# Kernel optimization log

Measured on AMD Instinct MI355X. Metric: run time of the kernel, lower is better.

## Reference

```python
import jax, jax.numpy as jnp
import numpy as np

E = 384      # hidden_dim
H = 8        # num_attention_heads
D = E // H   # head_dim = 48


def setup_inputs() -> dict:
    key = jax.random.key(0)
    ks = jax.random.split(key, 11)
    B, S = 4, 2048
    patch_embeds = jax.random.normal(ks[0], (B, S, E), dtype=jnp.float32)
    attention_mask = jax.random.randint(ks[1], (B, S), 0, 2).astype(bool)
    s = 1.0 / np.sqrt(E)
    Wq = jax.random.normal(ks[2], (E, E), dtype=jnp.float32) * s
    bq = jnp.zeros((E,), dtype=jnp.float32)
    Wk = jax.random.normal(ks[3], (E, E), dtype=jnp.float32) * s
    bk = jnp.zeros((E,), dtype=jnp.float32)
    Wv = jax.random.normal(ks[4], (E, E), dtype=jnp.float32) * s
    bv = jnp.zeros((E,), dtype=jnp.float32)
    Wo = jax.random.normal(ks[5], (E, E), dtype=jnp.float32) * s
    bo = jnp.zeros((E,), dtype=jnp.float32)
    return {"patch_embeds": patch_embeds, "attention_mask": attention_mask,
            "Wq": Wq, "bq": bq, "Wk": Wk, "bk": bk,
            "Wv": Wv, "bv": bv, "Wo": Wo, "bo": bo}


def reference(patch_embeds, attention_mask, Wq, bq, Wk, bk, Wv, bv, Wo, bo):
    B, S, _ = patch_embeds.shape
    scale = D ** (-0.5)
    # QKV projections (nn.Linear: x @ W.T + b); W stored as [out,in]
    q = patch_embeds @ Wq.T + bq
    k = patch_embeds @ Wk.T + bk
    v = patch_embeds @ Wv.T + bv
    # [B,S,E] -> [B,H,S,D]
    q = q.reshape(B, S, H, D).transpose(0, 2, 1, 3)
    k = k.reshape(B, S, H, D).transpose(0, 2, 1, 3)
    v = v.reshape(B, S, H, D).transpose(0, 2, 1, 3)
    # scaled dot-product attention with key mask (True = masked)
    scores = jnp.einsum('bhqd,bhkd->bhqk', q, k) * scale
    mask = attention_mask[:, None, None, :]  # [B,1,1,S]
    scores = jnp.where(mask, -jnp.inf, scores)
    weights = jax.nn.softmax(scores, axis=-1)
    out = jnp.einsum('bhqk,bhkd->bhqd', weights, v)
    out = out.transpose(0, 2, 1, 3).reshape(B, S, E)
    return out @ Wo.T + bo
```

## Files before the change

### kernel.cpp

```cpp
#include <hip/hip_runtime.h>
#include <math.h>

#define B_ 4
#define S_ 2048
#define E_ 384
#define H_ 8
#define D_ 48
#define M_ (B_*S_)
#define DP_ 64
constexpr float QK_SCALE = 0.14433756729740643f * 1.4426950408889634f;

typedef __attribute__((ext_vector_type(8))) short short8;
typedef __attribute__((ext_vector_type(4))) float f32x4;
typedef unsigned short u16;

__device__ inline u16 f2bf(float f) {
    unsigned u = __float_as_uint(f);
    return (u16)((u + 0x7FFFu + ((u >> 16) & 1u)) >> 16);
}
__device__ inline float bf2f(u16 h) { return __uint_as_float(((unsigned)h) << 16); }
__device__ inline unsigned pk2(float a, float b) {
    return (unsigned)f2bf(a) | ((unsigned)f2bf(b) << 16);
}
__device__ inline unsigned pk2_fast(float a, float b) {
#if __has_builtin(__builtin_amdgcn_perm)
    unsigned ua = __float_as_uint(a) + 0x8000u;
    unsigned ub = __float_as_uint(b) + 0x8000u;
    return __builtin_amdgcn_perm(ub, ua, 0x07060302u);
#else
    return pk2(a, b);
#endif
}
__device__ inline float fexp2(float x) {
#if __has_builtin(__builtin_amdgcn_exp2f)
    return __builtin_amdgcn_exp2f(x);
#else
    return exp2f(x);
#endif
}
__device__ inline void glld16(const void* g, void* l) {
    __builtin_amdgcn_global_load_lds((const __attribute__((address_space(1))) unsigned int*)g,
                                     (__attribute__((address_space(3))) unsigned int*)l, 16, 0, 0);
}

__global__ __launch_bounds__(256) void prep(const float4* __restrict__ x,
                                            const int* __restrict__ mask,
                                            const float4* __restrict__ wq,
                                            const float4* __restrict__ wk,
                                            const float4* __restrict__ wv,
                                            const float4* __restrict__ wo,
                                            uint2* __restrict__ xb,
                                            uint2* __restrict__ wb,
                                            u16* __restrict__ Qp, u16* __restrict__ Kp) {
    const int bx = blockIdx.x, t = threadIdx.x;
    if (bx < 3072) {
        int i = bx * 256 + t;
        float4 v = x[i];
        uint2 H;
        H.x = pk2(v.x, v.y);
        H.y = pk2(v.z, v.w);
        xb[i] = H;
    } else if (bx < 3072 + 144) {
        int i = (bx - 3072) * 256 + t;
        const int n4 = 36864;
        const float4* srcs[4] = {wq, wk, wv, wo};
        #pragma unroll
        for (int j = 0; j < 4; ++j) {
            float4 v = srcs[j][i];
            uint2 H;
            H.x = pk2(v.x, v.y);
            H.y = pk2(v.z, v.w);
            wb[(size_t)j * n4 + i] = H;
        }
    } else {
        int i = (bx - 3216) * 256 + t;
        int bh = i >> 11, s = i & 2047, b = bh >> 3;
        size_t off = ((size_t)bh * S_ + s) * DP_ + 48;
        uint4 qz = {0x00004300u, 0, 0, 0};
        uint4 kz = {mask[b * S_ + s] ? 0x0000BF80u : 0u, 0, 0, 0};
        uint4 z  = {0, 0, 0, 0};
        *reinterpret_cast<uint4*>(Qp + off)     = qz;
        *reinterpret_cast<uint4*>(Qp + off + 8) = z;
        *reinterpret_cast<uint4*>(Kp + off)     = kz;
        *reinterpret_cast<uint4*>(Kp + off + 8) = z;
    }
}

__global__ __launch_bounds__(256) void gemm_qkv3(const u16* __restrict__ xb,
                                                 const u16* __restrict__ wb,
                                                 const float* __restrict__ bq,
                                                 const float* __restrict__ bk,
                                                 const float* __restrict__ bv,
                                                 u16* __restrict__ Qp, u16* __restrict__ Kp,
                                                 u16* __restrict__ Vtp) {
    __shared__ u16 smem[4 * 4096];
    u16* As = smem;

    const int t = threadIdx.x, w = t >> 6, lane = t & 63;
    const int ln = lane & 15, quad = lane >> 4;
    const int gr = lane >> 3;
    const int gc = (lane & 7) ^ gr;
    const int m0 = blockIdx.x * 64;
    const int n0 = blockIdx.y * 64;
    const int b  = m0 >> 11;

    f32x4 acc[3][4];
    #pragma unroll
    for (int j = 0; j < 3; ++j)
        #pragma unroll
        for (int nt = 0; nt < 4; ++nt)
            acc[j][nt] = (f32x4){0.f, 0.f, 0.f, 0.f};

    for (int kk = 0; kk < 384; kk += 64) {
        __syncthreads();
        #pragma unroll
        for (int i = 0; i < 2; ++i) {
            int r0 = w * 16 + i * 8;
            glld16(xb + (size_t)(m0 + r0 + gr) * E_ + kk + gc * 8, As + r0 * 64);
        }
        #pragma unroll
        for (int j = 0; j < 3; ++j)
            #pragma unroll
            for (int i = 0; i < 2; ++i) {
                int r0 = w * 16 + i * 8;
                glld16(wb + (size_t)j * 147456 + (size_t)(n0 + r0 + gr) * E_ + kk + gc * 8,
                       smem + (1 + j) * 4096 + r0 * 64);
            }
        __syncthreads();

        #pragma unroll
        for (int ks = 0; ks < 2; ++ks) {
            const int slot = (ks * 4 + quad) ^ (ln & 7);
            short8 ah = *reinterpret_cast<const short8*>(&As[(w * 16 + ln) * 64 + slot * 8]);
            #pragma unroll
            for (int j = 0; j < 3; ++j) {
                const u16* Wsj = smem + (1 + j) * 4096;
                #pragma unroll
                for (int nt = 0; nt < 4; ++nt) {
                    short8 wf = *reinterpret_cast<const short8*>(&Wsj[(nt * 16 + ln) * 64 + slot * 8]);
                    acc[j][nt] = __builtin_amdgcn_mfma_f32_16x16x32_bf16(ah, wf, acc[j][nt], 0, 0, 0);
                }
            }
        }
    }

    {
        const int s_base = (m0 & 2047) + w * 16 + quad * 4;
        #pragma unroll
        for (int nt = 0; nt < 4; ++nt) {
            const int col = n0 + nt * 16 + ln;
            const int h   = (col * 683) >> 15;
            const int d   = col - h * 48;
            const float bc = bv[col];
            u16* dst = Vtp + ((size_t)(b * 8 + h) * 48 + d) * 2048;
            uint2 pk;
            pk.x = pk2(acc[2][nt][0] + bc, acc[2][nt][1] + bc);
            pk.y = pk2(acc[2][nt][2] + bc, acc[2][nt][3] + bc);
            *reinterpret_cast<uint2*>(dst + s_base) = pk;
        }
    }

    u16* TrQ = smem;
    u16* TrK = smem + 64 * 76;
    __syncthreads();
    #pragma unroll
    for (int nt = 0; nt < 4; ++nt) {
        const int col = n0 + nt * 16 + ln;
        const float bcq = bq[col], bck = bk[col];
        #pragma unroll
        for (int r = 0; r < 4; ++r) {
            int row = w * 16 + quad * 4 + r;
            TrQ[row * 76 + nt * 16 + ln] = f2bf((acc[0][nt][r] + bcq) * QK_SCALE);
            TrK[row * 76 + nt * 16 + ln] = f2bf(acc[1][nt][r] + bck);
        }
    }
    __syncthreads();
    {
        const int row = t >> 2, quarter = t & 3;
        const int s   = (m0 & 2047) + row;
        #pragma unroll
        for (int c = 0; c < 2; ++c) {
            int gcol = n0 + quarter * 16 + c * 8;
            int h = (gcol * 683) >> 15;
            int d = gcol - h * 48;
            size_t off = ((size_t)(b * 8 + h) * 2048 + s) * DP_ + d;
            *reinterpret_cast<uint4*>(Qp + off) =
                *reinterpret_cast<const uint4*>(&TrQ[row * 76 + quarter * 16 + c * 8]);
            *reinterpret_cast<uint4*>(Kp + off) =
                *reinterpret_cast<const uint4*>(&TrK[row * 76 + quarter * 16 + c * 8]);
        }
    }
}

__global__ __launch_bounds__(256) void gemm_out(const u16* __restrict__ ab,
                                                const u16* __restrict__ wb,
                                                const float* __restrict__ bo, float* __restrict__ out) {
    __shared__ u16 smem[2 * 4096 + 2 * 4096];
    u16* As = smem;
    u16* Ws = smem + 2 * 4096;
    const int t = threadIdx.x, w = t >> 6, lane = t & 63;
    const int ln = lane & 15, quad = lane >> 4;
    const int gr = lane >> 3;
    const int gc = (lane & 7) ^ gr;
    const int m0 = blockIdx.x * 64, n0 = blockIdx.y * 64;
    const u16* wh = wb + (size_t)3 * 147456;

    f32x4 acc[4];
    #pragma unroll
    for (int nt = 0; nt < 4; ++nt) acc[nt] = (f32x4){0.f, 0.f, 0.f, 0.f};

    auto stage = [&](int bf, int kk) {
        #pragma unroll
        for (int i = 0; i < 2; ++i) {
            int r0 = w * 16 + i * 8;
            glld16(ab + (size_t)(m0 + r0 + gr) * E_ + kk + gc * 8, As + bf * 4096 + r0 * 64);
            glld16(wh + (size_t)(n0 + r0 + gr) * E_ + kk + gc * 8, Ws + bf * 4096 + r0 * 64);
        }
    };

    stage(0, 0);
    __syncthreads();
    #pragma unroll
    for (int it = 0; it < 6; ++it) {
        const int cur = it & 1;
        if (it < 5) stage(cur ^ 1, (it + 1) * 64);
        const u16* Ab = As + cur * 4096;
        const u16* Wb = Ws + cur * 4096;
        #pragma unroll
        for (int ks = 0; ks < 2; ++ks) {
            const int slot = (ks * 4 + quad) ^ (ln & 7);
            short8 ah = *reinterpret_cast<const short8*>(&Ab[(w * 16 + ln) * 64 + slot * 8]);
            #pragma unroll
            for (int nt = 0; nt < 4; ++nt) {
                short8 wf = *reinterpret_cast<const short8*>(&Wb[(nt * 16 + ln) * 64 + slot * 8]);
                acc[nt] = __builtin_amdgcn_mfma_f32_16x16x32_bf16(ah, wf, acc[nt], 0, 0, 0);
            }
        }
        __syncthreads();
    }

    #pragma unroll
    for (int nt = 0; nt < 4; ++nt) {
        const int col = n0 + nt * 16 + ln;
        const float bc = bo[col];
        #pragma unroll
        for (int r = 0; r < 4; ++r) {
            size_t row = (size_t)(m0 + w * 16 + quad * 4 + r);
            out[row * E_ + col] = acc[nt][r] + bc;
        }
    }
}

__global__ __launch_bounds__(256, 2) void attn_mfma(const u16* __restrict__ Qp,
                                                    const u16* __restrict__ Kp,
                                                    const u16* __restrict__ Vtp,
                                                    u16* __restrict__ AO) {
    __shared__ __align__(16) u16 QPs[128 * 64];
    __shared__ __align__(16) u16 Ksh[2][64 * 64];
    __shared__ __align__(16) u16 Vt[2][48 * 64];
    __shared__ float linv[4][32];

    const int t    = threadIdx.x;
    const int w    = t >> 6;
    const int lane = t & 63;
    const int ln   = lane & 15;
    const int quad = lane >> 4;
    const int gr   = lane >> 3;
    const int gc   = (lane & 7) ^ gr;
    const int bh   = blockIdx.x;
    const int q0   = blockIdx.y * 128;
    const int b    = bh >> 3, h = bh & 7;
    const int cb   = h * 48;
    const size_t rb = (size_t)b * S_;

    const u16* Qsrc = Qp  + ((size_t)bh * S_ + q0) * DP_;
    const u16* Ksrc = Kp  + (size_t)bh * S_ * DP_;
    const u16* Vsrc = Vtp + (size_t)bh * 48 * 2048;

    const int swz0 = ((quad    ) ^ (ln & 7)) << 3;
    const int swz1 = ((4 + quad) ^ (ln & 7)) << 3;
    const u16* kA[2][2], *vA[2][2];
    #pragma unroll
    for (int bf = 0; bf < 2; ++bf) {
        kA[bf][0] = &Ksh[bf][ln * 64 + swz0];
        kA[bf][1] = &Ksh[bf][ln * 64 + swz1];
        vA[bf][0] = &Vt[bf][ln * 64 + swz0];
        vA[bf][1] = &Vt[bf][ln * 64 + swz1];
    }
    int qrow[2];
    const u16 *pR[2][2];
    u16* pW[2][4];
    #pragma unroll
    for (int qt = 0; qt < 2; ++qt) {
        qrow[qt] = (w * 32 + qt * 16 + ln) * 64;
        pR[qt][0] = &QPs[qrow[qt] + swz0];
        pR[qt][1] = &QPs[qrow[qt] + swz1];
        #pragma unroll
        for (int Mt = 0; Mt < 4; ++Mt)
            pW[qt][Mt] = &QPs[qrow[qt] +
                ((((Mt * 2 + (quad >> 1)) ^ (ln & 7)) << 3) | ((quad & 1) << 2))];
    }

    auto stage = [&](int bf, int kt) {
        const int k0 = kt * 64;
        glld16(Ksrc + (size_t)(k0 + w * 16 + gr) * DP_ + gc * 8,     &Ksh[bf][(w * 16) * 64]);
        glld16(Ksrc + (size_t)(k0 + w * 16 + 8 + gr) * DP_ + gc * 8, &Ksh[bf][(w * 16 + 8) * 64]);
        if (w < 3) {
            glld16(Vsrc + (size_t)(w * 16 + gr) * 2048 + k0 + gc * 8,     &Vt[bf][(w * 16) * 64]);
            glld16(Vsrc + (size_t)(w * 16 + 8 + gr) * 2048 + k0 + gc * 8, &Vt[bf][(w * 16 + 8) * 64]);
        }
    };

    #pragma unroll
    for (int i = 0; i < 4; ++i) {
        int r0 = w * 32 + i * 8;
        glld16(Qsrc + (size_t)(r0 + gr) * DP_ + gc * 8, &QPs[r0 * 64]);
    }
    stage(0, 0);
    __syncthreads();

    short8 qf[2][2];
    #pragma unroll
    for (int qt = 0; qt < 2; ++qt) {
        qf[qt][0] = *reinterpret_cast<const short8*>(pR[qt][0]);
        qf[qt][1] = *reinterpret_cast<const short8*>(pR[qt][1]);
    }

    f32x4 o[2][3];
    #pragma unroll
    for (int qt = 0; qt < 2; ++qt)
        #pragma unroll
        for (int nt = 0; nt < 3; ++nt) o[qt][nt] = (f32x4){0.f, 0.f, 0.f, 0.f};
    float lq[2] = {0.f, 0.f};

    auto body = [&](int cur, int nxt, int ktn) {
        if (ktn < 32) stage(nxt, ktn);

        f32x4 sc[4][2];
        #pragma unroll
        for (int Mt = 0; Mt < 4; ++Mt) {
            short8 kf0 = *reinterpret_cast<const short8*>(kA[cur][0] + Mt * 1024);
            short8 kf1 = *reinterpret_cast<const short8*>(kA[cur][1] + Mt * 1024);
            #pragma unroll
            for (int qt = 0; qt < 2; ++qt) {
                f32x4 a0 = __builtin_amdgcn_mfma_f32_16x16x32_bf16(kf0, qf[qt][0], (f32x4){0.f,0.f,0.f,0.f}, 0, 0, 0);
                sc[Mt][qt] = __builtin_amdgcn_mfma_f32_16x16x32_bf16(kf1, qf[qt][1], a0, 0, 0, 0);
            }
        }

        #pragma unroll
        for (int qt = 0; qt < 2; ++qt)
            #pragma unroll
            for (int Mt = 0; Mt < 4; ++Mt) {
                float p0 = fexp2(sc[Mt][qt][0]);
                float p1 = fexp2(sc[Mt][qt][1]);
                float p2 = fexp2(sc[Mt][qt][2]);
                float p3 = fexp2(sc[Mt][qt][3]);
                lq[qt] += (p0 + p1) + (p2 + p3);
                uint2 pk;
                pk.x = pk2_fast(p0, p1);
                pk.y = pk2_fast(p2, p3);
                *reinterpret_cast<uint2*>(pW[qt][Mt]) = pk;
            }

        short8 pa[2][2];
        #pragma unroll
        for (int qt = 0; qt < 2; ++qt) {
            pa[qt][0] = *reinterpret_cast<const short8*>(pR[qt][0]);
            pa[qt][1] = *reinterpret_cast<const short8*>(pR[qt][1]);
        }
        #pragma unroll
        for (int nt = 0; nt < 3; ++nt) {
            short8 vb0 = *reinterpret_cast<const short8*>(vA[cur][0] + nt * 1024);
            short8 vb1 = *reinterpret_cast<const short8*>(vA[cur][1] + nt * 1024);
            #pragma unroll
            for (int qt = 0; qt < 2; ++qt) {
                o[qt][nt] = __builtin_amdgcn_mfma_f32_16x16x32_bf16(pa[qt][0], vb0, o[qt][nt], 0, 0, 0);
                o[qt][nt] = __builtin_amdgcn_mfma_f32_16x16x32_bf16(pa[qt][1], vb1, o[qt][nt], 0, 0, 0);
            }
        }
        __syncthreads();
    };

    for (int kt = 0; kt < 32; kt += 2) {
        body(0, 1, kt + 1);
        body(1, 0, kt + 2);
    }

    #pragma unroll
    for (int qt = 0; qt < 2; ++qt) {
        float l = lq[qt];
        l += __shfl_xor(l, 16);
        l += __shfl_xor(l, 32);
        if (quad == 0) linv[w][qt * 16 + ln] = 1.0f / l;
    }
    __syncthreads();
    #pragma unroll
    for (int qt = 0; qt < 2; ++qt) {
        f32x4 il = *reinterpret_cast<const f32x4*>(&linv[w][qt * 16 + quad * 4]);
        #pragma unroll
        for (int nt = 0; nt < 3; ++nt)
            #pragma unroll
            for (int r = 0; r < 4; ++r) {
                size_t row = rb + q0 + w * 32 + qt * 16 + quad * 4 + r;
                size_t idx = row * E_ + cb + nt * 16 + ln;
                AO[idx] = f2bf(o[qt][nt][r] * il[r]);
            }
    }
}

extern "C" void kernel_launch(void* const* d_in, const int* in_sizes, int n_in,
                              void* d_out, int out_size, void* d_ws, size_t ws_size,
                              hipStream_t stream) {
    (void)in_sizes; (void)n_in; (void)out_size; (void)ws_size;
    const float* x    = (const float*)d_in[0];
    const int*   mask = (const int*)  d_in[1];
    const float* Wq   = (const float*)d_in[2];
    const float* bq   = (const float*)d_in[3];
    const float* Wk   = (const float*)d_in[4];
    const float* bk   = (const float*)d_in[5];
    const float* Wv   = (const float*)d_in[6];
    const float* bv   = (const float*)d_in[7];
    const float* Wo   = (const float*)d_in[8];
    const float* bo   = (const float*)d_in[9];

    const size_t NELEM = (size_t)M_ * E_;
    const size_t WELEM = (size_t)E_ * E_;
    const size_t PEL   = (size_t)B_ * H_ * S_ * DP_;
    u16* ws = (u16*)d_ws;
    u16* xb  = ws;
    u16* wb  = xb + NELEM;
    u16* Qp  = wb + 4 * WELEM;
    u16* Kp  = Qp + PEL;
    u16* Vtp = Kp + PEL;
    u16* AO  = xb;

    dim3 blk(256);
    prep<<<dim3(3472), blk, 0, stream>>>(
        (const float4*)x, mask,
        (const float4*)Wq, (const float4*)Wk, (const float4*)Wv, (const float4*)Wo,
        (uint2*)xb, (uint2*)wb, Qp, Kp);

    gemm_qkv3<<<dim3(M_ / 64, 6), blk, 0, stream>>>(xb, wb, bq, bk, bv, Qp, Kp, Vtp);

    attn_mfma<<<dim3(B_ * H_, S_ / 128), blk, 0, stream>>>(Qp, Kp, Vtp, AO);

    gemm_out<<<dim3(M_ / 64, 6), blk, 0, stream>>>(AO, wb, bo, (float*)d_out);
}
```

Measured before the change: 145.1 us.

## Split attention block across 8 waves with 16 query rows each

Result: slower. 148.9 us (+2.6%).

```diff
diff --git a/kernel.cpp b/kernel.cpp
--- a/kernel.cpp
+++ b/kernel.cpp
@@ -251,14 +251,14 @@
     }
 }
 
-__global__ __launch_bounds__(256, 2) void attn_mfma(const u16* __restrict__ Qp,
+__global__ __launch_bounds__(512, 4) void attn_mfma(const u16* __restrict__ Qp,
                                                     const u16* __restrict__ Kp,
                                                     const u16* __restrict__ Vtp,
                                                     u16* __restrict__ AO) {
     __shared__ __align__(16) u16 QPs[128 * 64];
     __shared__ __align__(16) u16 Ksh[2][64 * 64];
     __shared__ __align__(16) u16 Vt[2][48 * 64];
-    __shared__ float linv[4][32];
+    __shared__ float linv[8][16];
 
     const int t    = threadIdx.x;
     const int w    = t >> 6;
@@ -287,97 +287,74 @@
         vA[bf][0] = &Vt[bf][ln * 64 + swz0];
         vA[bf][1] = &Vt[bf][ln * 64 + swz1];
     }
-    int qrow[2];
-    const u16 *pR[2][2];
-    u16* pW[2][4];
-    #pragma unroll
-    for (int qt = 0; qt < 2; ++qt) {
-        qrow[qt] = (w * 32 + qt * 16 + ln) * 64;
-        pR[qt][0] = &QPs[qrow[qt] + swz0];
-        pR[qt][1] = &QPs[qrow[qt] + swz1];
-        #pragma unroll
-        for (int Mt = 0; Mt < 4; ++Mt)
-            pW[qt][Mt] = &QPs[qrow[qt] +
-                ((((Mt * 2 + (quad >> 1)) ^ (ln & 7)) << 3) | ((quad & 1) << 2))];
-    }
+    const int qrow = (w * 16 + ln) * 64;
+    const u16* pR[2];
+    u16* pW[4];
+    pR[0] = &QPs[qrow + swz0];
+    pR[1] = &QPs[qrow + swz1];
+    #pragma unroll
+    for (int Mt = 0; Mt < 4; ++Mt)
+        pW[Mt] = &QPs[qrow +
+            ((((Mt * 2 + (quad >> 1)) ^ (ln & 7)) << 3) | ((quad & 1) << 2))];
 
     auto stage = [&](int bf, int kt) {
         const int k0 = kt * 64;
-        glld16(Ksrc + (size_t)(k0 + w * 16 + gr) * DP_ + gc * 8,     &Ksh[bf][(w * 16) * 64]);
-        glld16(Ksrc + (size_t)(k0 + w * 16 + 8 + gr) * DP_ + gc * 8, &Ksh[bf][(w * 16 + 8) * 64]);
-        if (w < 3) {
-            glld16(Vsrc + (size_t)(w * 16 + gr) * 2048 + k0 + gc * 8,     &Vt[bf][(w * 16) * 64]);
-            glld16(Vsrc + (size_t)(w * 16 + 8 + gr) * 2048 + k0 + gc * 8, &Vt[bf][(w * 16 + 8) * 64]);
-        }
+        glld16(Ksrc + (size_t)(k0 + w * 8 + gr) * DP_ + gc * 8, &Ksh[bf][(w * 8) * 64]);
+        if (w < 6)
+            glld16(Vsrc + (size_t)(w * 8 + gr) * 2048 + k0 + gc * 8, &Vt[bf][(w * 8) * 64]);
     };
 
     #pragma unroll
-    for (int i = 0; i < 4; ++i) {
-        int r0 = w * 32 + i * 8;
+    for (int i = 0; i < 2; ++i) {
+        int r0 = w * 16 + i * 8;
         glld16(Qsrc + (size_t)(r0 + gr) * DP_ + gc * 8, &QPs[r0 * 64]);
     }
     stage(0, 0);
     __syncthreads();
 
-    short8 qf[2][2];
-    #pragma unroll
-    for (int qt = 0; qt < 2; ++qt) {
-        qf[qt][0] = *reinterpret_cast<const short8*>(pR[qt][0]);
-        qf[qt][1] = *reinterpret_cast<const short8*>(pR[qt][1]);
-    }
-
-    f32x4 o[2][3];
-    #pragma unroll
-    for (int qt = 0; qt < 2; ++qt)
-        #pragma unroll
-        for (int nt = 0; nt < 3; ++nt) o[qt][nt] = (f32x4){0.f, 0.f, 0.f, 0.f};
-    float lq[2] = {0.f, 0.f};
+    short8 qf[2];
+    qf[0] = *reinterpret_cast<const short8*>(pR[0]);
+    qf[1] = *reinterpret_cast<const short8*>(pR[1]);
+
+    f32x4 o[3];
+    #pragma unroll
+    for (int nt = 0; nt < 3; ++nt) o[nt] = (f32x4){0.f, 0.f, 0.f, 0.f};
+    float lq = 0.f;
 
     auto body = [&](int cur, int nxt, int ktn) {
         if (ktn < 32) stage(nxt, ktn);
 
-        f32x4 sc[4][2];
+        f32x4 sc[4];
         #pragma unroll
         for (int Mt = 0; Mt < 4; ++Mt) {
             short8 kf0 = *reinterpret_cast<const short8*>(kA[cur][0] + Mt * 1024);
             short8 kf1 = *reinterpret_cast<const short8*>(kA[cur][1] + Mt * 1024);
-            #pragma unroll
-            for (int qt = 0; qt < 2; ++qt) {
-                f32x4 a0 = __builtin_amdgcn_mfma_f32_16x16x32_bf16(kf0, qf[qt][0], (f32x4){0.f,0.f,0.f,0.f}, 0, 0, 0);
-                sc[Mt][qt] = __builtin_amdgcn_mfma_f32_16x16x32_bf16(kf1, qf[qt][1], a0, 0, 0, 0);
-            }
-        }
-
-        #pragma unroll
-        for (int qt = 0; qt < 2; ++qt)
-            #pragma unroll
-            for (int Mt = 0; Mt < 4; ++Mt) {
-                float p0 = fexp2(sc[Mt][qt][0]);
-                float p1 = fexp2(sc[Mt][qt][1]);
-                float p2 = fexp2(sc[Mt][qt][2]);
-                float p3 = fexp2(sc[Mt][qt][3]);
-                lq[qt] += (p0 + p1) + (p2 + p3);
-                uint2 pk;
-                pk.x = pk2_fast(p0, p1);
-                pk.y = pk2_fast(p2, p3);
-                *reinterpret_cast<uint2*>(pW[qt][Mt]) = pk;
-            }
-
-        short8 pa[2][2];
-        #pragma unroll
-        for (int qt = 0; qt < 2; ++qt) {
-            pa[qt][0] = *reinterpret_cast<const short8*>(pR[qt][0]);
-            pa[qt][1] = *reinterpret_cast<const short8*>(pR[qt][1]);
-        }
+            f32x4 a0 = __builtin_amdgcn_mfma_f32_16x16x32_bf16(kf0, qf[0], (f32x4){0.f,0.f,0.f,0.f}, 0, 0, 0);
+            sc[Mt] = __builtin_amdgcn_mfma_f32_16x16x32_bf16(kf1, qf[1], a0, 0, 0, 0);
+        }
+
+        #pragma unroll
+        for (int Mt = 0; Mt < 4; ++Mt) {
+            float p0 = fexp2(sc[Mt][0]);
+            float p1 = fexp2(sc[Mt][1]);
+            float p2 = fexp2(sc[Mt][2]);
+            float p3 = fexp2(sc[Mt][3]);
+            lq += (p0 + p1) + (p2 + p3);
+            uint2 pk;
+            pk.x = pk2_fast(p0, p1);
+            pk.y = pk2_fast(p2, p3);
+            *reinterpret_cast<uint2*>(pW[Mt]) = pk;
+        }
+
+        short8 pa[2];
+        pa[0] = *reinterpret_cast<const short8*>(pR[0]);
+        pa[1] = *reinterpret_cast<const short8*>(pR[1]);
         #pragma unroll
         for (int nt = 0; nt < 3; ++nt) {
             short8 vb0 = *reinterpret_cast<const short8*>(vA[cur][0] + nt * 1024);
             short8 vb1 = *reinterpret_cast<const short8*>(vA[cur][1] + nt * 1024);
-            #pragma unroll
-            for (int qt = 0; qt < 2; ++qt) {
-                o[qt][nt] = __builtin_amdgcn_mfma_f32_16x16x32_bf16(pa[qt][0], vb0, o[qt][nt], 0, 0, 0);
-                o[qt][nt] = __builtin_amdgcn_mfma_f32_16x16x32_bf16(pa[qt][1], vb1, o[qt][nt], 0, 0, 0);
-            }
+            o[nt] = __builtin_amdgcn_mfma_f32_16x16x32_bf16(pa[0], vb0, o[nt], 0, 0, 0);
+            o[nt] = __builtin_amdgcn_mfma_f32_16x16x32_bf16(pa[1], vb1, o[nt], 0, 0, 0);
         }
         __syncthreads();
     };
@@ -387,24 +364,22 @@
         body(1, 0, kt + 2);
     }
 
-    #pragma unroll
-    for (int qt = 0; qt < 2; ++qt) {
-        float l = lq[qt];
+    {
+        float l = lq;
         l += __shfl_xor(l, 16);
         l += __shfl_xor(l, 32);
-        if (quad == 0) linv[w][qt * 16 + ln] = 1.0f / l;
+        if (quad == 0) linv[w][ln] = 1.0f / l;
     }
     __syncthreads();
-    #pragma unroll
-    for (int qt = 0; qt < 2; ++qt) {
-        f32x4 il = *reinterpret_cast<const f32x4*>(&linv[w][qt * 16 + quad * 4]);
+    {
+        f32x4 il = *reinterpret_cast<const f32x4*>(&linv[w][quad * 4]);
         #pragma unroll
         for (int nt = 0; nt < 3; ++nt)
             #pragma unroll
             for (int r = 0; r < 4; ++r) {
-                size_t row = rb + q0 + w * 32 + qt * 16 + quad * 4 + r;
+                size_t row = rb + q0 + w * 16 + quad * 4 + r;
                 size_t idx = row * E_ + cb + nt * 16 + ln;
-                AO[idx] = f2bf(o[qt][nt][r] * il[r]);
+                AO[idx] = f2bf(o[nt][r] * il[r]);
             }
     }
 }
@@ -443,7 +418,7 @@
 
     gemm_qkv3<<<dim3(M_ / 64, 6), blk, 0, stream>>>(xb, wb, bq, bk, bv, Qp, Kp, Vtp);
 
-    attn_mfma<<<dim3(B_ * H_, S_ / 128), blk, 0, stream>>>(Qp, Kp, Vtp, AO);
+    attn_mfma<<<dim3(B_ * H_, S_ / 128), dim3(512), 0, stream>>>(Qp, Kp, Vtp, AO);
 
     gemm_out<<<dim3(M_ / 64, 6), blk, 0, stream>>>(AO, wb, bo, (float*)d_out);
 }
```
